# Performance work log

Measured on AMD Instinct MI355X. Metric: run time of the kernel, lower is better.

## Reference

```python
import jax, jax.numpy as jnp
import numpy as np

QUERY_DIM, FEAT_DIM, HID_DIM, OUT_DIM = 512, 2048, 512, 512
B, L, S, T = 8, 128, 100, 100


def setup_inputs() -> dict:
    key = jax.random.key(0)
    ks = jax.random.split(key, 9)
    d = {
        "query": jax.random.normal(ks[0], (B, L, QUERY_DIM), jnp.float32),
        "src": jax.random.normal(ks[1], (B, S, FEAT_DIM), jnp.float32),
        "trg": jax.random.normal(ks[2], (B, T, FEAT_DIM), jnp.float32),
        # params (LinearAct == Linear + identity act); src/trg projections share weights
        "Wq": jax.random.normal(ks[3], (QUERY_DIM, HID_DIM), jnp.float32) / np.sqrt(QUERY_DIM),
        "bq": jnp.zeros((HID_DIM,), jnp.float32),
        "Ws": jax.random.normal(ks[4], (FEAT_DIM, HID_DIM), jnp.float32) / np.sqrt(FEAT_DIM),
        "bs": jnp.zeros((HID_DIM,), jnp.float32),
        "Wo": jax.random.normal(ks[5], (HID_DIM + QUERY_DIM, OUT_DIM), jnp.float32) / np.sqrt(HID_DIM + QUERY_DIM),
        "bo": jnp.zeros((OUT_DIM,), jnp.float32),
    }
    return d


def reference(query, src, trg, Wq, bq, Ws, bs, Wo, bo):
    b, l, _ = query.shape
    s = src.shape[1]
    t = trg.shape[1]
    q = query @ Wq + bq          # b,l,k
    s_key = src @ Ws + bs        # b,s,k
    t_key = trg @ Ws + bs        # b,t,k
    hid = q.shape[-1]
    # score[b,l,s,t] = q . (s_key - t_key)/sqrt(2) / sqrt(hid) -- decomposed, no b,s,t,k tensor
    qs = jnp.einsum('blk,bsk->bls', q, s_key)
    qt = jnp.einsum('blk,btk->blt', q, t_key)
    score = (qs[:, :, :, None] - qt[:, :, None, :]) / jnp.sqrt(jnp.asarray(2.0 * hid, q.dtype))
    w = jax.nn.softmax(score.reshape(b, l, s * t), axis=-1).reshape(b, l, s, t)
    # ctx = sum_{s,t} w * (s_key - t_key)/sqrt(2), decomposed via marginals
    ws = w.sum(axis=3)           # b,l,s
    wt = w.sum(axis=2)           # b,l,t
    ctx = (jnp.einsum('bls,bsk->blk', ws, s_key) - jnp.einsum('blt,btk->blk', wt, t_key)) / jnp.sqrt(jnp.asarray(2.0, q.dtype))
    x = jnp.concatenate([query, ctx], axis=-1) @ Wo + bo
    return x
```

## Files before the change

kernel.cpp:

```cpp
#include <hip/hip_runtime.h>
#include <math.h>


typedef __attribute__((ext_vector_type(8))) short s16x8;
typedef __attribute__((ext_vector_type(4))) float f32x4;

__device__ __forceinline__ unsigned short f2bf(float f) {
    unsigned int u = __float_as_uint(f);
    return (unsigned short)((u + 0x7fffu + ((u >> 16) & 1u)) >> 16);
}

__global__ __launch_bounds__(256) void k_prep(
    const float* __restrict__ query, const float* __restrict__ src,
    const float* __restrict__ trg, const float* __restrict__ Wq,
    const float* __restrict__ Ws, const float* __restrict__ Wo,
    const float* __restrict__ bs, const float* __restrict__ bo,
    unsigned short* __restrict__ qbf, unsigned short* __restrict__ aout,
    unsigned short* __restrict__ abf, unsigned short* __restrict__ WqT,
    unsigned short* __restrict__ WsT, unsigned short* __restrict__ WoT,
    float* __restrict__ keys, float* __restrict__ out, float* __restrict__ sc) {
    __shared__ float tile[32][33];
    const int bid = blockIdx.x, t = threadIdx.x;

    if (bid < 3712) {
        const int idx = bid * 256 + t;
        if (idx < 131072) {
            float4 v = *(const float4*)(query + (size_t)idx * 4);
            ushort4 o = make_ushort4(f2bf(v.x), f2bf(v.y), f2bf(v.z), f2bf(v.w));
            *(ushort4*)(qbf + (size_t)idx * 4) = o;
            const int flat = idx * 4, m = flat >> 9, c = flat & 511;
            *(ushort4*)(aout + (size_t)m * 1024 + c) = o;
        } else if (idx < 540672) {
            const int i = idx - 131072;
            float4 v = *(const float4*)(src + (size_t)i * 4);
            *(ushort4*)(abf + (size_t)i * 4) =
                make_ushort4(f2bf(v.x), f2bf(v.y), f2bf(v.z), f2bf(v.w));
        } else {
            const int i = idx - 540672;
            float4 v = *(const float4*)(trg + (size_t)i * 4);
            *(ushort4*)(abf + 1638400 + (size_t)i * 4) =
                make_ushort4(f2bf(v.x), f2bf(v.y), f2bf(v.z), f2bf(v.w));
        }
    } else if (bid < 5504) {
        const int id = bid - 3712;
        const float* W; unsigned short* O; int K, tk, tn;
        if (id < 256)       { W = Wq; O = WqT; K = 512;  tk = id >> 4;          tn = id & 15; }
        else if (id < 1280) { W = Ws; O = WsT; K = 2048; tk = (id - 256) >> 4;  tn = (id - 256) & 15; }
        else                { W = Wo; O = WoT; K = 1024; tk = (id - 1280) >> 4; tn = (id - 1280) & 15; }
        const int row = t >> 3, c4 = (t & 7) * 4;
        float4 v = *(const float4*)(W + (size_t)(tk * 32 + row) * 512 + tn * 32 + c4);
        tile[row][c4 + 0] = v.x; tile[row][c4 + 1] = v.y;
        tile[row][c4 + 2] = v.z; tile[row][c4 + 3] = v.w;
        __syncthreads();
        ushort4 o = make_ushort4(f2bf(tile[c4 + 0][row]), f2bf(tile[c4 + 1][row]),
                                 f2bf(tile[c4 + 2][row]), f2bf(tile[c4 + 3][row]));
        *(ushort4*)(O + (size_t)(tn * 32 + row) * K + tk * 32 + c4) = o;
    } else if (bid < 6304) {
        const int f = ((bid - 5504) * 256 + t) * 4;
        *(float4*)(keys + f) = *(const float4*)(bs + (f & 511));
    } else if (bid < 6816) {
        const int f = ((bid - 6304) * 256 + t) * 4;
        *(float4*)(out + f) = *(const float4*)(bo + (f & 511));
    } else {
        const int f = ((bid - 6816) * 256 + t) * 4;
        *(float4*)(sc + f) = make_float4(0.f, 0.f, 0.f, 0.f);
    }
}


__device__ __forceinline__ void gemm64_atomic(
    const unsigned short* __restrict__ A, const unsigned short* __restrict__ BT,
    float* __restrict__ C, int m0, int n0, int K, int N, int kbase, int kiters,
    unsigned short* As, unsigned short* Bs) {
    const int t = threadIdx.x;
    const int lane = t & 63, wid = t >> 6;
    const int wm = (wid & 1) * 32, wn = (wid >> 1) * 32;
    const int lr = lane & 15, lq = lane >> 4;
    const int r = t >> 3, c8 = (t & 7) * 8;

    s16x8 ra0, ra1, rb0, rb1;
#define LD64(kt)                                                           \
    ra0 = *(const s16x8*)(A  + (size_t)(m0 + r)      * K + (kt) + c8);     \
    ra1 = *(const s16x8*)(A  + (size_t)(m0 + r + 32) * K + (kt) + c8);     \
    rb0 = *(const s16x8*)(BT + (size_t)(n0 + r)      * K + (kt) + c8);     \
    rb1 = *(const s16x8*)(BT + (size_t)(n0 + r + 32) * K + (kt) + c8);

    f32x4 acc[2][2] = {};
    LD64(kbase);
    for (int it = 0; it < kiters; it++) {
        __syncthreads();
        *(s16x8*)&As[r * 72 + c8]        = ra0;
        *(s16x8*)&As[(r + 32) * 72 + c8] = ra1;
        *(s16x8*)&Bs[r * 72 + c8]        = rb0;
        *(s16x8*)&Bs[(r + 32) * 72 + c8] = rb1;
        __syncthreads();
        if (it + 1 < kiters) { LD64(kbase + (it + 1) * 64); }
#pragma unroll
        for (int s = 0; s < 2; s++) {
            s16x8 a0 = *(const s16x8*)&As[(wm + lr) * 72      + s * 32 + lq * 8];
            s16x8 a1 = *(const s16x8*)&As[(wm + 16 + lr) * 72 + s * 32 + lq * 8];
            s16x8 b0 = *(const s16x8*)&Bs[(wn + lr) * 72      + s * 32 + lq * 8];
            s16x8 b1 = *(const s16x8*)&Bs[(wn + 16 + lr) * 72 + s * 32 + lq * 8];
            acc[0][0] = __builtin_amdgcn_mfma_f32_16x16x32_bf16(a0, b0, acc[0][0], 0, 0, 0);
            acc[0][1] = __builtin_amdgcn_mfma_f32_16x16x32_bf16(a0, b1, acc[0][1], 0, 0, 0);
            acc[1][0] = __builtin_amdgcn_mfma_f32_16x16x32_bf16(a1, b0, acc[1][0], 0, 0, 0);
            acc[1][1] = __builtin_amdgcn_mfma_f32_16x16x32_bf16(a1, b1, acc[1][1], 0, 0, 0);
        }
    }
#undef LD64
#pragma unroll
    for (int i = 0; i < 2; i++)
#pragma unroll
        for (int j = 0; j < 2; j++) {
            const int col = n0 + wn + j * 16 + lr;
            const int row = m0 + wm + i * 16 + lq * 4;
#pragma unroll
            for (int rr = 0; rr < 4; rr++)
                unsafeAtomicAdd(&C[(size_t)(row + rr) * N + col], acc[i][j][rr]);
        }
}

template <int MODE>
__device__ __forceinline__ void gemm32(
    const unsigned short* __restrict__ A, const unsigned short* __restrict__ BT,
    const float* __restrict__ bias, void* __restrict__ Cv,
    int m0, int n0, int K, int N, int kbase, int kiters,
    unsigned short* As, unsigned short* Bs) {
    const int t = threadIdx.x;
    const int lane = t & 63, wid = t >> 6;
    const int wm = (wid & 1) * 16, wn = (wid >> 1) * 32;
    const int lr = lane & 15, lq = lane >> 4;
    const int r = t >> 3, c8 = (t & 7) * 8;

    s16x8 ra, rb0, rb1;
#define LD32(kt)                                                           \
    ra  = *(const s16x8*)(A  + (size_t)(m0 + r)      * K + (kt) + c8);     \
    rb0 = *(const s16x8*)(BT + (size_t)(n0 + r)      * K + (kt) + c8);     \
    rb1 = *(const s16x8*)(BT + (size_t)(n0 + r + 32) * K + (kt) + c8);

    f32x4 acc[2] = {};
    LD32(kbase);
    for (int it = 0; it < kiters; it++) {
        __syncthreads();
        *(s16x8*)&As[r * 72 + c8]        = ra;
        *(s16x8*)&Bs[r * 72 + c8]        = rb0;
        *(s16x8*)&Bs[(r + 32) * 72 + c8] = rb1;
        __syncthreads();
        if (it + 1 < kiters) { LD32(kbase + (it + 1) * 64); }
#pragma unroll
        for (int s = 0; s < 2; s++) {
            s16x8 a0 = *(const s16x8*)&As[(wm + lr) * 72      + s * 32 + lq * 8];
            s16x8 b0 = *(const s16x8*)&Bs[(wn + lr) * 72      + s * 32 + lq * 8];
            s16x8 b1 = *(const s16x8*)&Bs[(wn + 16 + lr) * 72 + s * 32 + lq * 8];
            acc[0] = __builtin_amdgcn_mfma_f32_16x16x32_bf16(a0, b0, acc[0], 0, 0, 0);
            acc[1] = __builtin_amdgcn_mfma_f32_16x16x32_bf16(a0, b1, acc[1], 0, 0, 0);
        }
    }
#undef LD32
#pragma unroll
    for (int j = 0; j < 2; j++) {
        const int col = n0 + wn + j * 16 + lr;
        const int row = m0 + wm + lq * 4;
        if (MODE == 1) {
            float* C = (float*)Cv;
#pragma unroll
            for (int rr = 0; rr < 4; rr++)
                unsafeAtomicAdd(&C[(size_t)(row + rr) * N + col], acc[j][rr]);
        } else if (MODE == 0) {
            float* C = (float*)Cv;
            const float bv = bias[col];
#pragma unroll
            for (int rr = 0; rr < 4; rr++)
                C[(size_t)(row + rr) * N + col] = acc[j][rr] + bv;
        } else {
            unsigned short* C = (unsigned short*)Cv;
            const float bv = bias[col];
#pragma unroll
            for (int rr = 0; rr < 4; rr++)
                C[(size_t)(row + rr) * N + col] = f2bf(acc[j][rr] + bv);
        }
    }
}

__global__ __launch_bounds__(256) void k_stageB(
    const unsigned short* __restrict__ qbf, const unsigned short* __restrict__ abf,
    const unsigned short* __restrict__ WqT, const unsigned short* __restrict__ WsT,
    const float* __restrict__ bq, unsigned short* __restrict__ qh,
    float* __restrict__ keys) {
    __shared__ __align__(16) unsigned short As[64 * 72];
    __shared__ __align__(16) unsigned short Bs[64 * 72];
    const int bid = blockIdx.x;
    if (bid < 800) {
        const int c = bid / 200, rem = bid % 200;
        const int mt = rem >> 3, nt = rem & 7;
        gemm64_atomic(abf, WsT, keys, mt * 64, nt * 64, 2048, 512, c * 512, 8, As, Bs);
    } else {
        const int r = bid - 800;
        const int mt = r >> 3, nt = r & 7;
        gemm32<2>(qbf, WqT, bq, qh, mt * 32, nt * 64, 512, 512, 0, 8, As, Bs);
    }
}

__global__ __launch_bounds__(256) void k_scgemm(
    const unsigned short* __restrict__ qh, const float* __restrict__ keys,
    float* __restrict__ sc) {
    __shared__ __align__(16) unsigned short As[32 * 72];
    __shared__ __align__(16) unsigned short Bs[64 * 72];
    const int bid = blockIdx.x;
    const int c = bid >> 7, rem = bid & 127;
    const int mt = rem >> 2, nt = rem & 3;
    const int m0 = mt * 32, b = mt >> 2, n0 = nt * 64;
    const int kbase = c * 256;
    const int t = threadIdx.x;
    const int lane = t & 63, wid = t >> 6;
    const int wm = (wid & 1) * 16, wn = (wid >> 1) * 32;
    const int lr = lane & 15, lq = lane >> 4;
    const int r = t >> 3, c8 = (t & 7) * 8;

    const int nA = n0 + r, nB = n0 + r + 32;
    int kr0 = (nA < 128) ? (b * 100 + nA) : (800 + b * 100 + (nA - 128));
    int kr1 = (nB < 128) ? (b * 100 + nB) : (800 + b * 100 + (nB - 128));
    kr0 = kr0 > 1599 ? 1599 : kr0;
    kr1 = kr1 > 1599 ? 1599 : kr1;

    s16x8 ra, rb0, rb1;
    auto cvt8 = [](const float* p) {
        float4 u = *(const float4*)p, w = *(const float4*)(p + 4);
        s16x8 o;
        o[0] = (short)f2bf(u.x); o[1] = (short)f2bf(u.y);
        o[2] = (short)f2bf(u.z); o[3] = (short)f2bf(u.w);
        o[4] = (short)f2bf(w.x); o[5] = (short)f2bf(w.y);
        o[6] = (short)f2bf(w.z); o[7] = (short)f2bf(w.w);
        return o;
    };
#define LDSC(kt)                                                   \
    ra  = *(const s16x8*)(qh + (size_t)(m0 + r) * 512 + (kt) + c8); \
    rb0 = cvt8(keys + (size_t)kr0 * 512 + (kt) + c8);               \
    rb1 = cvt8(keys + (size_t)kr1 * 512 + (kt) + c8);

    f32x4 acc[2] = {};
    LDSC(kbase);
    for (int it = 0; it < 4; it++) {
        __syncthreads();
        *(s16x8*)&As[r * 72 + c8]        = ra;
        *(s16x8*)&Bs[r * 72 + c8]        = rb0;
        *(s16x8*)&Bs[(r + 32) * 72 + c8] = rb1;
        __syncthreads();
        if (it < 3) { LDSC(kbase + (it + 1) * 64); }
#pragma unroll
        for (int s = 0; s < 2; s++) {
            s16x8 a0 = *(const s16x8*)&As[(wm + lr) * 72      + s * 32 + lq * 8];
            s16x8 b0 = *(const s16x8*)&Bs[(wn + lr) * 72      + s * 32 + lq * 8];
            s16x8 b1 = *(const s16x8*)&Bs[(wn + 16 + lr) * 72 + s * 32 + lq * 8];
            acc[0] = __builtin_amdgcn_mfma_f32_16x16x32_bf16(a0, b0, acc[0], 0, 0, 0);
            acc[1] = __builtin_amdgcn_mfma_f32_16x16x32_bf16(a0, b1, acc[1], 0, 0, 0);
        }
    }
#undef LDSC
#pragma unroll
    for (int j = 0; j < 2; j++) {
        const int col = n0 + wn + j * 16 + lr;
        const int row = m0 + wm + lq * 4;
        const float scale = (col >= 128) ? -(1.0f / 32.0f) : (1.0f / 32.0f);
#pragma unroll
        for (int rr = 0; rr < 4; rr++)
            unsafeAtomicAdd(&sc[(size_t)(row + rr) * 256 + col],
                            acc[j][rr] * scale);
    }
}

__global__ __launch_bounds__(256) void k_ctx(
    const float* __restrict__ sc, const float* __restrict__ keys,
    unsigned short* __restrict__ aout) {
    __shared__ float wbuf[200 * 33];
    __shared__ float Bs[40 * 32];

    const int t = threadIdx.x;
    const int b = blockIdx.y;
    const int n0 = blockIdx.x * 32;
    const int l0 = blockIdx.z * 32;
    const int wave = t >> 6, lane = t & 63;

    for (int i = 0; i < 8; i++) {
        const int li = wave * 8 + i;
        const float4 v = *(const float4*)(
            sc + (size_t)(b * 128 + l0 + li) * 256 + lane * 4);
        const float vv[4] = {v.x, v.y, v.z, v.w};
        const int c0 = lane * 4;
        float mS = -1e30f, mT = -1e30f;
#pragma unroll
        for (int j = 0; j < 4; j++) {
            const int col = c0 + j;
            if (col < 100) mS = fmaxf(mS, vv[j]);
            if (col >= 128 && col < 228) mT = fmaxf(mT, vv[j]);
        }
#pragma unroll
        for (int off = 32; off > 0; off >>= 1) {
            mS = fmaxf(mS, __shfl_xor(mS, off));
            mT = fmaxf(mT, __shfl_xor(mT, off));
        }
        float eS[4], eT[4], sS = 0.f, sT = 0.f;
#pragma unroll
        for (int j = 0; j < 4; j++) {
            const int col = c0 + j;
            eS[j] = (col < 100) ? __expf(vv[j] - mS) : 0.f;
            eT[j] = (col >= 128 && col < 228) ? __expf(vv[j] - mT) : 0.f;
            sS += eS[j]; sT += eT[j];
        }
#pragma unroll
        for (int off = 32; off > 0; off >>= 1) {
            sS += __shfl_xor(sS, off);
            sT += __shfl_xor(sT, off);
        }
        const float iS = 1.f / sS, iT = 1.f / sT;
#pragma unroll
        for (int j = 0; j < 4; j++) {
            const int col = c0 + j;
            if (col < 100) wbuf[col * 33 + li] = eS[j] * iS;
            if (col >= 128 && col < 228)
                wbuf[(100 + col - 128) * 33 + li] = eT[j] * iT;
        }
    }
    __syncthreads();

    const int tx = t & 7, ty = t >> 3;
    float rB[5];
    auto loadB = [&](int kbase) {
#pragma unroll
        for (int e = 0; e < 5; e++) {
            const int idx = t + e * 256;
            const int k = idx >> 5, j = idx & 31;
            const int kk = kbase + k;
            rB[e] = (kk < 100)
                ?  keys[(size_t)(b * 100 + kk) * 512 + n0 + j]
                : -keys[(size_t)(800 + b * 100 + (kk - 100)) * 512 + n0 + j];
        }
    };

    float acc[4] = {};
    loadB(0);
    for (int c5 = 0; c5 < 5; c5++) {
        __syncthreads();
#pragma unroll
        for (int e = 0; e < 5; e++) {
            const int idx = t + e * 256;
            Bs[idx] = rB[e];
        }
        __syncthreads();
        if (c5 < 4) loadB((c5 + 1) * 40);
#pragma unroll 8
        for (int k = 0; k < 40; k++) {
            const float ar = wbuf[(c5 * 40 + k) * 33 + ty];
            float br[4];
            *(float4*)br = *(const float4*)&Bs[k * 32 + tx * 4];
#pragma unroll
            for (int j = 0; j < 4; j++) acc[j] = fmaf(ar, br[j], acc[j]);
        }
    }

    const float s2 = 0.70710678118654752f;
    const int m = b * 128 + l0 + ty;
    ushort4 o = make_ushort4(f2bf(acc[0] * s2), f2bf(acc[1] * s2),
                             f2bf(acc[2] * s2), f2bf(acc[3] * s2));
    *(ushort4*)(aout + (size_t)m * 1024 + 512 + n0 + tx * 4) = o;
}

__global__ __launch_bounds__(256) void k_out(
    const unsigned short* __restrict__ aout, const unsigned short* __restrict__ WoT,
    float* __restrict__ out) {
    __shared__ __align__(16) unsigned short As[64 * 72];
    __shared__ __align__(16) unsigned short Bs[64 * 72];
    const int bid = blockIdx.x;
    const int c = bid >> 8, rem = bid & 255;
    const int mt = rem >> 3, nt = rem & 7;
    gemm32<1>(aout, WoT, nullptr, out, mt * 32, nt * 64, 1024, 512,
              c * 512, 8, As, Bs);
}


extern "C" void kernel_launch(void* const* d_in, const int* in_sizes, int n_in,
                              void* d_out, int out_size, void* d_ws, size_t ws_size,
                              hipStream_t stream) {
    const float* query = (const float*)d_in[0];
    const float* src   = (const float*)d_in[1];
    const float* trg   = (const float*)d_in[2];
    const float* Wq    = (const float*)d_in[3];
    const float* bq    = (const float*)d_in[4];
    const float* Ws    = (const float*)d_in[5];
    const float* bs    = (const float*)d_in[6];
    const float* Wo    = (const float*)d_in[7];
    const float* bo    = (const float*)d_in[8];
    float* out = (float*)d_out;

    float* keys = (float*)d_ws;
    float* sc   = keys + 819200;
    unsigned short* qbf = (unsigned short*)(sc + 262144);
    unsigned short* qh  = qbf + 524288;
    unsigned short* abf = qh  + 524288;
    unsigned short* aout= abf + 3276800;
    unsigned short* wqt = aout + 1048576;
    unsigned short* wst = wqt  + 262144;
    unsigned short* wot = wst  + 1048576;

    k_prep<<<7072, 256, 0, stream>>>(query, src, trg, Wq, Ws, Wo, bs, bo,
                                     qbf, aout, abf, wqt, wst, wot,
                                     keys, out, sc);
    k_stageB<<<1056, 256, 0, stream>>>(qbf, abf, wqt, wst, bq, qh, keys);
    k_scgemm<<<256, 256, 0, stream>>>(qh, keys, sc);
    k_ctx<<<dim3(16, 8, 4), 256, 0, stream>>>(sc, keys, aout);
    k_out<<<512, 256, 0, stream>>>(aout, wot, out);
}
```

Before: 132.7 us.

## Split output GEMM by input half, drop split-K atomics and redundant query copy

The query-half of the output projection (query @ Wo[:512]) now runs in the stage-B kernel alongside the key and q projections, writing out with the bias directly. k_out only does the context half and accumulates atomically, so the zeroing and bias init of out and sc in the prep kernel are gone. The q projection reads the bf16 query straight from the concatenated aout buffer, so the separate qbf copy is dropped. Split-K factors are halved in the key GEMM and removed in the score GEMM (plain stores instead of atomics), giving fewer blocks with longer K loops and less parallelism.

```diff
diff --git a/kernel.cpp b/kernel.cpp
--- a/kernel.cpp
+++ b/kernel.cpp
@@ -14,11 +14,10 @@
     const float* __restrict__ query, const float* __restrict__ src,
     const float* __restrict__ trg, const float* __restrict__ Wq,
     const float* __restrict__ Ws, const float* __restrict__ Wo,
-    const float* __restrict__ bs, const float* __restrict__ bo,
-    unsigned short* __restrict__ qbf, unsigned short* __restrict__ aout,
-    unsigned short* __restrict__ abf, unsigned short* __restrict__ WqT,
-    unsigned short* __restrict__ WsT, unsigned short* __restrict__ WoT,
-    float* __restrict__ keys, float* __restrict__ out, float* __restrict__ sc) {
+    const float* __restrict__ bs,
+    unsigned short* __restrict__ aout, unsigned short* __restrict__ abf,
+    unsigned short* __restrict__ WqT, unsigned short* __restrict__ WsT,
+    unsigned short* __restrict__ WoT, float* __restrict__ keys) {
     __shared__ float tile[32][33];
     const int bid = blockIdx.x, t = threadIdx.x;
 
@@ -27,7 +26,6 @@
         if (idx < 131072) {
             float4 v = *(const float4*)(query + (size_t)idx * 4);
             ushort4 o = make_ushort4(f2bf(v.x), f2bf(v.y), f2bf(v.z), f2bf(v.w));
-            *(ushort4*)(qbf + (size_t)idx * 4) = o;
             const int flat = idx * 4, m = flat >> 9, c = flat & 511;
             *(ushort4*)(aout + (size_t)m * 1024 + c) = o;
         } else if (idx < 540672) {
@@ -55,15 +53,9 @@
         ushort4 o = make_ushort4(f2bf(tile[c4 + 0][row]), f2bf(tile[c4 + 1][row]),
                                  f2bf(tile[c4 + 2][row]), f2bf(tile[c4 + 3][row]));
         *(ushort4*)(O + (size_t)(tn * 32 + row) * K + tk * 32 + c4) = o;
-    } else if (bid < 6304) {
+    } else {
         const int f = ((bid - 5504) * 256 + t) * 4;
         *(float4*)(keys + f) = *(const float4*)(bs + (f & 511));
-    } else if (bid < 6816) {
-        const int f = ((bid - 6304) * 256 + t) * 4;
-        *(float4*)(out + f) = *(const float4*)(bo + (f & 511));
-    } else {
-        const int f = ((bid - 6816) * 256 + t) * 4;
-        *(float4*)(sc + f) = make_float4(0.f, 0.f, 0.f, 0.f);
     }
 }
 
@@ -124,7 +116,7 @@
 __device__ __forceinline__ void gemm32(
     const unsigned short* __restrict__ A, const unsigned short* __restrict__ BT,
     const float* __restrict__ bias, void* __restrict__ Cv,
-    int m0, int n0, int K, int N, int kbase, int kiters,
+    int m0, int n0, int KA, int KB, int N, int kbase, int kiters,
     unsigned short* As, unsigned short* Bs) {
     const int t = threadIdx.x;
     const int lane = t & 63, wid = t >> 6;
@@ -133,10 +125,10 @@
     const int r = t >> 3, c8 = (t & 7) * 8;
 
     s16x8 ra, rb0, rb1;
-#define LD32(kt)                                                           \
-    ra  = *(const s16x8*)(A  + (size_t)(m0 + r)      * K + (kt) + c8);     \
-    rb0 = *(const s16x8*)(BT + (size_t)(n0 + r)      * K + (kt) + c8);     \
-    rb1 = *(const s16x8*)(BT + (size_t)(n0 + r + 32) * K + (kt) + c8);
+#define LD32(kt)                                                            \
+    ra  = *(const s16x8*)(A  + (size_t)(m0 + r)      * KA + (kt) + c8);     \
+    rb0 = *(const s16x8*)(BT + (size_t)(n0 + r)      * KB + (kt) + c8);     \
+    rb1 = *(const s16x8*)(BT + (size_t)(n0 + r + 32) * KB + (kt) + c8);
 
     f32x4 acc[2] = {};
     LD32(kbase);
@@ -183,21 +175,29 @@
 }
 
 __global__ __launch_bounds__(256) void k_stageB(
-    const unsigned short* __restrict__ qbf, const unsigned short* __restrict__ abf,
+    const unsigned short* __restrict__ aoutA, const unsigned short* __restrict__ abf,
     const unsigned short* __restrict__ WqT, const unsigned short* __restrict__ WsT,
-    const float* __restrict__ bq, unsigned short* __restrict__ qh,
-    float* __restrict__ keys) {
+    const unsigned short* __restrict__ WoT, const float* __restrict__ bq,
+    const float* __restrict__ bo, unsigned short* __restrict__ qh,
+    float* __restrict__ keys, float* __restrict__ out) {
     __shared__ __align__(16) unsigned short As[64 * 72];
     __shared__ __align__(16) unsigned short Bs[64 * 72];
     const int bid = blockIdx.x;
-    if (bid < 800) {
+    if (bid < 400) {
         const int c = bid / 200, rem = bid % 200;
         const int mt = rem >> 3, nt = rem & 7;
-        gemm64_atomic(abf, WsT, keys, mt * 64, nt * 64, 2048, 512, c * 512, 8, As, Bs);
+        gemm64_atomic(abf, WsT, keys, mt * 64, nt * 64, 2048, 512,
+                      c * 1024, 16, As, Bs);
+    } else if (bid < 656) {
+        const int r = bid - 400;
+        const int mt = r >> 3, nt = r & 7;
+        gemm32<2>(aoutA, WqT, bq, qh, mt * 32, nt * 64, 1024, 512, 512,
+                  0, 8, As, Bs);
     } else {
-        const int r = bid - 800;
+        const int r = bid - 656;
         const int mt = r >> 3, nt = r & 7;
-        gemm32<2>(qbf, WqT, bq, qh, mt * 32, nt * 64, 512, 512, 0, 8, As, Bs);
+        gemm32<0>(aoutA, WoT, bo, out, mt * 32, nt * 64, 1024, 1024, 512,
+                  0, 8, As, Bs);
     }
 }
 
@@ -207,10 +207,8 @@
     __shared__ __align__(16) unsigned short As[32 * 72];
     __shared__ __align__(16) unsigned short Bs[64 * 72];
     const int bid = blockIdx.x;
-    const int c = bid >> 7, rem = bid & 127;
-    const int mt = rem >> 2, nt = rem & 3;
+    const int mt = bid >> 2, nt = bid & 3;
     const int m0 = mt * 32, b = mt >> 2, n0 = nt * 64;
-    const int kbase = c * 256;
     const int t = threadIdx.x;
     const int lane = t & 63, wid = t >> 6;
     const int wm = (wid & 1) * 16, wn = (wid >> 1) * 32;
@@ -233,20 +231,20 @@
         o[6] = (short)f2bf(w.z); o[7] = (short)f2bf(w.w);
         return o;
     };
-#define LDSC(kt)                                                   \
+#define LDSC(kt)                                                    \
     ra  = *(const s16x8*)(qh + (size_t)(m0 + r) * 512 + (kt) + c8); \
     rb0 = cvt8(keys + (size_t)kr0 * 512 + (kt) + c8);               \
     rb1 = cvt8(keys + (size_t)kr1 * 512 + (kt) + c8);
 
     f32x4 acc[2] = {};
-    LDSC(kbase);
-    for (int it = 0; it < 4; it++) {
+    LDSC(0);
+    for (int it = 0; it < 8; it++) {
         __syncthreads();
         *(s16x8*)&As[r * 72 + c8]        = ra;
         *(s16x8*)&Bs[r * 72 + c8]        = rb0;
         *(s16x8*)&Bs[(r + 32) * 72 + c8] = rb1;
         __syncthreads();
-        if (it < 3) { LDSC(kbase + (it + 1) * 64); }
+        if (it < 7) { LDSC((it + 1) * 64); }
 #pragma unroll
         for (int s = 0; s < 2; s++) {
             s16x8 a0 = *(const s16x8*)&As[(wm + lr) * 72      + s * 32 + lq * 8];
@@ -264,8 +262,7 @@
         const float scale = (col >= 128) ? -(1.0f / 32.0f) : (1.0f / 32.0f);
 #pragma unroll
         for (int rr = 0; rr < 4; rr++)
-            unsafeAtomicAdd(&sc[(size_t)(row + rr) * 256 + col],
-                            acc[j][rr] * scale);
+            sc[(size_t)(row + rr) * 256 + col] = acc[j][rr] * scale;
     }
 }
 
@@ -371,10 +368,9 @@
     __shared__ __align__(16) unsigned short As[64 * 72];
     __shared__ __align__(16) unsigned short Bs[64 * 72];
     const int bid = blockIdx.x;
-    const int c = bid >> 8, rem = bid & 255;
-    const int mt = rem >> 3, nt = rem & 7;
-    gemm32<1>(aout, WoT, nullptr, out, mt * 32, nt * 64, 1024, 512,
-              c * 512, 8, As, Bs);
+    const int mt = bid >> 3, nt = bid & 7;
+    gemm32<1>(aout, WoT, nullptr, out, mt * 32, nt * 64, 1024, 1024, 512,
+              512, 8, As, Bs);
 }
 
 
@@ -394,19 +390,18 @@
 
     float* keys = (float*)d_ws;
     float* sc   = keys + 819200;
-    unsigned short* qbf = (unsigned short*)(sc + 262144);
-    unsigned short* qh  = qbf + 524288;
+    unsigned short* qh  = (unsigned short*)(sc + 262144);
     unsigned short* abf = qh  + 524288;
     unsigned short* aout= abf + 3276800;
     unsigned short* wqt = aout + 1048576;
     unsigned short* wst = wqt  + 262144;
     unsigned short* wot = wst  + 1048576;
 
-    k_prep<<<7072, 256, 0, stream>>>(query, src, trg, Wq, Ws, Wo, bs, bo,
-                                     qbf, aout, abf, wqt, wst, wot,
-                                     keys, out, sc);
-    k_stageB<<<1056, 256, 0, stream>>>(qbf, abf, wqt, wst, bq, qh, keys);
-    k_scgemm<<<256, 256, 0, stream>>>(qh, keys, sc);
+    k_prep<<<6304, 256, 0, stream>>>(query, src, trg, Wq, Ws, Wo, bs,
+                                     aout, abf, wqt, wst, wot, keys);
+    k_stageB<<<912, 256, 0, stream>>>(aout, abf, wqt, wst, wot, bq, bo,
+                                      qh, keys, out);
+    k_scgemm<<<128, 256, 0, stream>>>(qh, keys, sc);
     k_ctx<<<dim3(16, 8, 4), 256, 0, stream>>>(sc, keys, aout);
-    k_out<<<512, 256, 0, stream>>>(aout, wot, out);
-}
+    k_out<<<256, 256, 0, stream>>>(aout, wot, out);
+}
```

New measurement: 132.6 us. About the same (-0.1%).
